# Performance work log

Hardware: AMD Instinct MI355X
Metric: run time of the kernel (lower is better)

The kernel has to match this reference:

```python
import jax, jax.numpy as jnp
import numpy as np

EMBED = 2048
HEADS = 32
HEAD_DIM = EMBED // HEADS
Q_BITS = 4
Q_MAX = 2 ** (Q_BITS - 1) - 1  # 7
DECOMP = 8
CHUNK = 256


def _sym_qdq(x, scale):
    # sym_quant followed by sym_dequant (float32 math, clamp to [-8, 7])
    s = jnp.clip(jnp.abs(scale), 1e-9, None)
    return jnp.clip(jnp.round(x / s), -(Q_MAX + 1), Q_MAX) * s


def _quant_weight(w):
    # per-output-channel symmetric int4 quant-dequant of weight [out, in]
    w = w.astype(jnp.float32)
    s = jnp.max(jnp.abs(w), axis=-1, keepdims=True) / Q_MAX
    return _sym_qdq(w, s)


def _chunk_decompose(x2d):
    """Tender chunked activation quantization.
    Splits rows into chunks of CHUNK, subtracts per-chunk channel bias,
    groups channels into DECOMP scale groups by their column max, and
    applies per-group int4 quant-dequant. Vectorized over the DECOMP groups
    (the masks partition channels, so a per-channel scale gather is exact).
    """
    T, H = x2d.shape
    chunks = (T + CHUNK - 1) // CHUNK
    pad = chunks * CHUNK - T
    xp = jnp.pad(x2d, ((0, pad), (0, 0))).reshape(chunks, CHUNK, H).astype(jnp.float32)
    ch_bias = (jnp.max(xp, axis=1, keepdims=True) + jnp.min(xp, axis=1, keepdims=True)) / 2
    xz = xp - ch_bias                                   # [chunks, CHUNK, H]
    tmax = jnp.max(jnp.abs(xz), axis=(1, 2))            # [chunks]
    cmax = jnp.max(jnp.abs(xz), axis=1)                 # [chunks, H]
    # thresholds t_i = tmax / 2^(DECOMP-1-i), ascending in i
    thr = tmax[:, None] / (2.0 ** jnp.arange(DECOMP - 1, -1, -1, dtype=jnp.float32))
    # group index: i=0 if cmax<=t0, else first i with t_{i-1} < cmax <= t_i
    idx = jnp.sum(cmax[:, :, None] > thr[:, None, : DECOMP - 1], axis=-1)  # [chunks, H]
    scale = tmax[:, None] / (2.0 ** (DECOMP - 1 - idx).astype(jnp.float32)) / Q_MAX
    result = _sym_qdq(xz, scale[:, None, :])            # [chunks, CHUNK, H]
    return result, ch_bias, T


def reference(hidden_states, q_weight, k_weight, v_weight, o_weight,
              q_bias, k_bias, v_bias, o_bias):
    bsz, tgt, H = hidden_states.shape
    # int4 dequantized weights, transposed for right-multiply
    WQ = _quant_weight(q_weight).T
    WK = _quant_weight(k_weight).T
    WV = _quant_weight(v_weight).T
    WO = _quant_weight(o_weight).T

    result, ch_bias, n = _chunk_decompose(hidden_states.reshape(bsz * tgt, H))

    def proj(w_orig, w_dq_t, b):
        # bias-corrected dequant GEMM: per-chunk channel bias uses the
        # ORIGINAL (fp) weight, quantized residual uses the int4 weight
        y = result @ w_dq_t + ch_bias @ w_orig.astype(jnp.float32).T
        return y.reshape(-1, H)[:n] + b

    scaling = HEAD_DIM ** -0.5
    Q = (proj(q_weight, WQ, q_bias) * scaling).reshape(bsz, tgt, HEADS, HEAD_DIM)
    K = proj(k_weight, WK, k_bias).reshape(bsz, tgt, HEADS, HEAD_DIM)
    V = proj(v_weight, WV, v_bias).reshape(bsz, tgt, HEADS, HEAD_DIM)

    # quant_mha == False path: plain attention
    attn = jnp.einsum('bqhd,bkhd->bhqk', Q, K)
    probs = jax.nn.softmax(attn, axis=-1)
    ctx = jnp.einsum('bhqk,bkhd->bqhd', probs, V).reshape(bsz * tgt, H)

    # output projection through the same chunked quant pipeline
    r2, cb2, n2 = _chunk_decompose(ctx)
    out = (r2 @ WO + cb2 @ o_weight.astype(jnp.float32).T).reshape(-1, H)[:n2] + o_bias
    return out.reshape(bsz, tgt, H)


def setup_inputs() -> dict:
    key = jax.random.key(0)
    ks = jax.random.split(key, 10)
    B, T = 2, 1024
    inp = {
        'hidden_states': jax.random.normal(ks[0], (B, T, EMBED), dtype=jnp.float32),
        'q_weight': jax.random.normal(ks[1], (EMBED, EMBED), dtype=jnp.float32) * 0.02,
        'k_weight': jax.random.normal(ks[2], (EMBED, EMBED), dtype=jnp.float32) * 0.02,
        'v_weight': jax.random.normal(ks[3], (EMBED, EMBED), dtype=jnp.float32) * 0.02,
        'o_weight': jax.random.normal(ks[4], (EMBED, EMBED), dtype=jnp.float32) * 0.02,
        'q_bias': jax.random.normal(ks[5], (EMBED,), dtype=jnp.float32) * 0.02,
        'k_bias': jax.random.normal(ks[6], (EMBED,), dtype=jnp.float32) * 0.02,
        'v_bias': jax.random.normal(ks[7], (EMBED,), dtype=jnp.float32) * 0.02,
        'o_bias': jax.random.normal(ks[8], (EMBED,), dtype=jnp.float32) * 0.02,
    }
    return inp
```

## Files before the change

kernel.cpp:

```cpp
#include <hip/hip_runtime.h>
#include <hip/hip_bf16.h>

typedef unsigned short u16;
typedef unsigned int u32;
typedef __attribute__((ext_vector_type(8))) short bs8;
typedef __attribute__((ext_vector_type(4))) float fx4;
typedef __attribute__((ext_vector_type(4))) float f4_t;
typedef __attribute__((ext_vector_type(4))) unsigned int u4_t;

#define HDIM 2048
#define NCH 8

__device__ inline u16 f2bf(float f) {
  __hip_bfloat16 h = __float2bfloat16(f);
  return __builtin_bit_cast(u16, h);
}
__device__ inline float bf2f(u16 u) {
  __hip_bfloat16 h = __builtin_bit_cast(__hip_bfloat16, u);
  return __bfloat162float(h);
}
__device__ inline float pow2i(int e) {
  return __builtin_bit_cast(float, (unsigned)((127 + e) << 23));
}
__device__ inline void gld_lds16(const void* g, void* l) {
  __builtin_amdgcn_global_load_lds((const __attribute__((address_space(1))) void*)g,
                                   (__attribute__((address_space(3))) void*)l, 16, 0, 0);
}

__global__ __launch_bounds__(256) void k_wquant_cbw(
    const float* __restrict__ w0, const float* __restrict__ w1,
    const float* __restrict__ w2, const float* __restrict__ bias,
    u16* __restrict__ wq, float* __restrict__ sw, float* __restrict__ cbw,
    int NC) {
  int o = blockIdx.x, t = threadIdx.x;
  const float* w = (o < 2048) ? w0 : ((o < 4096) ? w1 : w2);
  const float* wrow = w + (size_t)(o & 2047) * HDIM;
  const f4_t* row4 = (const f4_t*)wrow;
  f4_t x0 = row4[2 * t], x1 = row4[2 * t + 1];
  float am = 0.f;
#pragma unroll
  for (int j = 0; j < 4; j++) { am = fmaxf(am, fabsf(x0[j])); am = fmaxf(am, fabsf(x1[j])); }
#pragma unroll
  for (int m = 1; m < 64; m <<= 1) am = fmaxf(am, __shfl_xor(am, m));
  __shared__ float red[4];
  if ((t & 63) == 0) red[t >> 6] = am;
  __syncthreads();
  am = fmaxf(fmaxf(red[0], red[1]), fmaxf(red[2], red[3]));
  float s = fmaxf(am / 7.0f, 1e-9f);
  if (t == 0) sw[o] = s;
  bs8 ov;
#pragma unroll
  for (int j = 0; j < 4; j++) {
    float q0 = fminf(fmaxf(rintf(x0[j] / s), -8.f), 7.f);
    float q1 = fminf(fmaxf(rintf(x1[j] / s), -8.f), 7.f);
    ov[j]     = (short)f2bf(q0);
    ov[j + 4] = (short)f2bf(q1);
  }
  ((bs8*)(wq + (size_t)o * HDIM))[t] = ov;
  float acc[NCH];
#pragma unroll
  for (int c = 0; c < NCH; c++) {
    const f4_t* bc = (const f4_t*)(bias + (size_t)c * HDIM);
    f4_t b0 = bc[2 * t], b1 = bc[2 * t + 1];
    float a = 0.f;
#pragma unroll
    for (int j = 0; j < 4; j++) a += x0[j] * b0[j] + x1[j] * b1[j];
    acc[c] = a;
  }
  __shared__ float redc[NCH][4];
#pragma unroll
  for (int c = 0; c < NCH; c++) {
    float a = acc[c];
#pragma unroll
    for (int m = 1; m < 64; m <<= 1) a += __shfl_xor(a, m);
    if ((t & 63) == 0) redc[c][t >> 6] = a;
  }
  __syncthreads();
  if (t < NCH) cbw[t * NC + o] = redc[t][0] + redc[t][1] + redc[t][2] + redc[t][3];
}

__global__ __launch_bounds__(256) void k_stats(const float* __restrict__ x,
                                               float* __restrict__ biasO,
                                               float* __restrict__ cmaxO) {
  int ch = blockIdx.x >> 3;
  int c = ((blockIdx.x & 7) << 8) + threadIdx.x;
  const float* base = x + (size_t)ch * 256 * HDIM + c;
  float mx = -1e30f, mn = 1e30f;
  for (int r = 0; r < 256; r++) { float v = base[(size_t)r * HDIM]; mx = fmaxf(mx, v); mn = fminf(mn, v); }
  float bi = (mx + mn) * 0.5f;
  biasO[ch * HDIM + c] = bi;
  cmaxO[ch * HDIM + c] = fmaxf(mx - bi, bi - mn);
}

__global__ __launch_bounds__(256) void k_tscale(const float* __restrict__ cmax,
                                                float* __restrict__ scaleO,
                                                float* __restrict__ e2O,
                                                float* __restrict__ tcO) {
  int ch = blockIdx.x, t = threadIdx.x;
  const float* cr = cmax + ch * HDIM;
  float v[8];
  float mx = 0.f;
#pragma unroll
  for (int i = 0; i < 8; i++) { v[i] = cr[i * 256 + t]; mx = fmaxf(mx, v[i]); }
#pragma unroll
  for (int m = 1; m < 64; m <<= 1) mx = fmaxf(mx, __shfl_xor(mx, m));
  __shared__ float red[4];
  __shared__ float tms;
  if ((t & 63) == 0) red[t >> 6] = mx;
  __syncthreads();
  if (t == 0) tms = fmaxf(fmaxf(red[0], red[1]), fmaxf(red[2], red[3]));
  __syncthreads();
  float tmax = tms;
  if (t == 0) tcO[ch] = (tmax / 7.0f) * pow2i(-7);
#pragma unroll
  for (int i = 0; i < 8; i++) {
    int idx = 0;
#pragma unroll
    for (int k = 0; k < 7; k++) idx += (v[i] > tmax * pow2i(k - 7)) ? 1 : 0;
    float s = (tmax * pow2i(idx - 7)) / 7.0f;
    scaleO[ch * HDIM + i * 256 + t] = fmaxf(s, 1e-9f);
    e2O[ch * HDIM + i * 256 + t] = pow2i(idx);
  }
}

__global__ __launch_bounds__(256) void k_qdq(const float* __restrict__ x,
                                             const float* __restrict__ bias,
                                             const float* __restrict__ scale,
                                             const float* __restrict__ e2,
                                             u16* __restrict__ out) {
  int row = blockIdx.x, t = threadIdx.x;
  int ch = row >> 8;
  const f4_t* xr = (const f4_t*)(x + (size_t)row * HDIM);
  const f4_t* br = (const f4_t*)(bias + (size_t)ch * HDIM);
  const f4_t* sr = (const f4_t*)(scale + (size_t)ch * HDIM);
  const f4_t* er = (const f4_t*)(e2 + (size_t)ch * HDIM);
  f4_t x0 = xr[2 * t], x1 = xr[2 * t + 1];
  f4_t b0 = br[2 * t], b1 = br[2 * t + 1];
  f4_t s0 = sr[2 * t], s1 = sr[2 * t + 1];
  f4_t e0 = er[2 * t], e1 = er[2 * t + 1];
  bs8 ov;
#pragma unroll
  for (int j = 0; j < 4; j++) {
    float q0 = fminf(fmaxf(rintf((x0[j] - b0[j]) / s0[j]), -8.f), 7.f);
    ov[j] = (short)f2bf(q0 * e0[j]);
    float q1 = fminf(fmaxf(rintf((x1[j] - b1[j]) / s1[j]), -8.f), 7.f);
    ov[j + 4] = (short)f2bf(q1 * e1[j]);
  }
  ((bs8*)(out + (size_t)row * HDIM))[t] = ov;
}

__global__ __launch_bounds__(256) void k_gemm(
    const u16* __restrict__ A, const u16* __restrict__ B,
    float* __restrict__ o0, float* __restrict__ o1, float* __restrict__ o2,
    const float* __restrict__ cbw, int NC,
    const float* __restrict__ bb0, const float* __restrict__ bb1,
    const float* __restrict__ bb2,
    const float* __restrict__ tc, const float* __restrict__ sw,
    float scl0, float scl1, float scl2) {
  __shared__ u16 smA[128 * 32];
  __shared__ u16 smB[128 * 32];
  int tid = threadIdx.x;
  int wave = tid >> 6, lane = tid & 63;
  int wr = wave >> 1, wc = wave & 1;
  int row0 = blockIdx.y * 128, col0 = blockIdx.x * 128;
  int mat = col0 >> 11;
  float* out = (mat == 0) ? o0 : ((mat == 1) ? o1 : o2);
  const float* bias = (mat == 0) ? bb0 : ((mat == 1) ? bb1 : bb2);
  float scl = (mat == 0) ? scl0 : ((mat == 1) ? scl1 : scl2);
  int chunk = row0 >> 8;
  fx4 zz = {0.f, 0.f, 0.f, 0.f};
  fx4 acc[4][4];
#pragma unroll
  for (int m = 0; m < 4; m++)
#pragma unroll
    for (int n = 0; n < 4; n++) acc[m][n] = zz;

  int offB = wave * 1024 + lane * 16;
  int sr0 = offB >> 6;
  int sr1 = sr0 + 64;
  int sk = (lane & 3) << 3;
  char* ldsA0 = (char*)smA + wave * 1024;
  char* ldsA1 = (char*)smA + 4096 + wave * 1024;
  char* ldsB0 = (char*)smB + wave * 1024;
  char* ldsB1 = (char*)smB + 4096 + wave * 1024;
  const u16* Ab = A + (size_t)row0 * HDIM;
  const u16* Bb = B + (size_t)col0 * HDIM;

  int arow = wr * 64 + (lane & 15);
  int brow = wc * 64 + (lane & 15);
  int kByte = (lane >> 4) << 4;

  for (int kt = 0; kt < HDIM / 32; kt++) {
    int kb = kt * 32 + sk;
    gld_lds16(Ab + (size_t)sr0 * HDIM + kb, ldsA0);
    gld_lds16(Ab + (size_t)sr1 * HDIM + kb, ldsA1);
    gld_lds16(Bb + (size_t)sr0 * HDIM + kb, ldsB0);
    gld_lds16(Bb + (size_t)sr1 * HDIM + kb, ldsB1);
    __syncthreads();
    bs8 af[4], bfr[4];
#pragma unroll
    for (int m = 0; m < 4; m++)
      af[m] = *(const bs8*)((const char*)smA + (size_t)((arow + m * 16) * 64 + kByte));
#pragma unroll
    for (int n = 0; n < 4; n++)
      bfr[n] = *(const bs8*)((const char*)smB + (size_t)((brow + n * 16) * 64 + kByte));
#pragma unroll
    for (int m = 0; m < 4; m++)
#pragma unroll
      for (int n = 0; n < 4; n++)
        acc[m][n] = __builtin_amdgcn_mfma_f32_16x16x32_bf16(af[m], bfr[n], acc[m][n], 0, 0, 0);
    __syncthreads();
  }
  float tcv = tc[chunk];
  int colb = col0 + wc * 64 + (lane & 15);
  int rowb = row0 + wr * 64 + ((lane >> 4) << 2);
#pragma unroll
  for (int m = 0; m < 4; m++) {
#pragma unroll
    for (int n = 0; n < 4; n++) {
      int colg = colb + n * 16;
      int colL = colg - (mat << 11);
      float sc = tcv * sw[colg];
      float cb = cbw[chunk * NC + colg] + bias[colL];
#pragma unroll
      for (int j = 0; j < 4; j++) {
        int row = rowb + m * 16 + j;
        out[(size_t)row * HDIM + colL] = (acc[m][n][j] * sc + cb) * scl;
      }
    }
  }
}

__global__ __launch_bounds__(256) void k_gemm_sk(const u16* __restrict__ A,
                                                 const u16* __restrict__ B,
                                                 float* __restrict__ pbuf) {
  __shared__ u16 smA[128 * 32];
  __shared__ u16 smB[128 * 32];
  int tid = threadIdx.x;
  int wave = tid >> 6, lane = tid & 63;
  int wr = wave >> 1, wc = wave & 1;
  int row0 = blockIdx.y * 128, col0 = blockIdx.x * 128;
  int z = blockIdx.z;
  float* out = pbuf + (size_t)z * HDIM * HDIM;
  fx4 zz = {0.f, 0.f, 0.f, 0.f};
  fx4 acc[4][4];
#pragma unroll
  for (int m = 0; m < 4; m++)
#pragma unroll
    for (int n = 0; n < 4; n++) acc[m][n] = zz;

  int offB = wave * 1024 + lane * 16;
  int sr0 = offB >> 6;
  int sr1 = sr0 + 64;
  int sk = (lane & 3) << 3;
  char* ldsA0 = (char*)smA + wave * 1024;
  char* ldsA1 = (char*)smA + 4096 + wave * 1024;
  char* ldsB0 = (char*)smB + wave * 1024;
  char* ldsB1 = (char*)smB + 4096 + wave * 1024;
  const u16* Ab = A + (size_t)row0 * HDIM;
  const u16* Bb = B + (size_t)col0 * HDIM;

  int arow = wr * 64 + (lane & 15);
  int brow = wc * 64 + (lane & 15);
  int kByte = (lane >> 4) << 4;

  for (int kt = z * 32; kt < z * 32 + 32; kt++) {
    int kb = kt * 32 + sk;
    gld_lds16(Ab + (size_t)sr0 * HDIM + kb, ldsA0);
    gld_lds16(Ab + (size_t)sr1 * HDIM + kb, ldsA1);
    gld_lds16(Bb + (size_t)sr0 * HDIM + kb, ldsB0);
    gld_lds16(Bb + (size_t)sr1 * HDIM + kb, ldsB1);
    __syncthreads();
    bs8 af[4], bfr[4];
#pragma unroll
    for (int m = 0; m < 4; m++)
      af[m] = *(const bs8*)((const char*)smA + (size_t)((arow + m * 16) * 64 + kByte));
#pragma unroll
    for (int n = 0; n < 4; n++)
      bfr[n] = *(const bs8*)((const char*)smB + (size_t)((brow + n * 16) * 64 + kByte));
#pragma unroll
    for (int m = 0; m < 4; m++)
#pragma unroll
      for (int n = 0; n < 4; n++)
        acc[m][n] = __builtin_amdgcn_mfma_f32_16x16x32_bf16(af[m], bfr[n], acc[m][n], 0, 0, 0);
    __syncthreads();
  }
  int colb = col0 + wc * 64 + (lane & 15);
  int rowb = row0 + wr * 64 + ((lane >> 4) << 2);
#pragma unroll
  for (int m = 0; m < 4; m++)
#pragma unroll
    for (int n = 0; n < 4; n++)
#pragma unroll
      for (int j = 0; j < 4; j++)
        out[(size_t)(rowb + m * 16 + j) * HDIM + colb + n * 16] = acc[m][n][j];
}

__global__ __launch_bounds__(256) void k_fin(const float* __restrict__ p0,
                                             const float* __restrict__ p1,
                                             const float* __restrict__ cbw,
                                             const float* __restrict__ bias,
                                             const float* __restrict__ tc,
                                             const float* __restrict__ sw,
                                             float* __restrict__ out) {
  int row = blockIdx.x, t = threadIdx.x;
  int chunk = row >> 8;
  float tcv = tc[chunk];
  const f4_t* a = (const f4_t*)(p0 + (size_t)row * HDIM);
  const f4_t* b = (const f4_t*)(p1 + (size_t)row * HDIM);
  f4_t* o = (f4_t*)(out + (size_t)row * HDIM);
#pragma unroll
  for (int u = 0; u < 2; u++) {
    f4_t x = a[2 * t + u], y = b[2 * t + u];
    f4_t r;
#pragma unroll
    for (int j = 0; j < 4; j++) {
      int c = (2 * t + u) * 4 + j;
      float sc = tcv * sw[c];
      float cb = cbw[chunk * HDIM + c] + bias[c];
      r[j] = ((x[j] + y[j]) * sc + cb) * 1.0f;
    }
    o[2 * t + u] = r;
  }
}

__global__ __launch_bounds__(256) void k_split(const float* __restrict__ Kf,
                                               const float* __restrict__ Vf,
                                               u16* __restrict__ Khg,
                                               u16* __restrict__ Klg,
                                               u16* __restrict__ Vhg,
                                               u16* __restrict__ Vlg) {
  __shared__ u16 Th[4096], Tl[4096];
  int t = threadIdx.x;
  int ti = blockIdx.x & 15, h = (blockIdx.x >> 4) & 31, b = blockIdx.x >> 9;
  size_t rowStart = (size_t)b * 1024 + ti * 64;
  int colh = h * 64;
  size_t tbase = ((size_t)((b * 32 + h) * 16 + ti)) * 4096;
  int kr = t >> 2, d0 = (t & 3) << 4;
  int xk = (kr & 7) << 3;
  const float* kp = Kf + (rowStart + kr) * HDIM + colh + d0;
  const float* vp = Vf + (rowStart + kr) * HDIM + colh + d0;
  f4_t kv[4], vv[4];
#pragma unroll
  for (int qd = 0; qd < 4; qd++) { kv[qd] = *(const f4_t*)(kp + 4 * qd); vv[qd] = *(const f4_t*)(vp + 4 * qd); }
  bs8 h0, l0, h1, l1;
#pragma unroll
  for (int j = 0; j < 4; j++) {
    float x = kv[0][j]; u16 hh = f2bf(x); h0[j] = (short)hh; l0[j] = (short)f2bf(x - bf2f(hh));
    x = kv[1][j]; hh = f2bf(x); h0[j + 4] = (short)hh; l0[j + 4] = (short)f2bf(x - bf2f(hh));
    x = kv[2][j]; hh = f2bf(x); h1[j] = (short)hh; l1[j] = (short)f2bf(x - bf2f(hh));
    x = kv[3][j]; hh = f2bf(x); h1[j + 4] = (short)hh; l1[j + 4] = (short)f2bf(x - bf2f(hh));
  }
  *(bs8*)(Khg + tbase + kr * 64 + (d0 ^ xk)) = h0;
  *(bs8*)(Klg + tbase + kr * 64 + (d0 ^ xk)) = l0;
  *(bs8*)(Khg + tbase + kr * 64 + ((d0 + 8) ^ xk)) = h1;
  *(bs8*)(Klg + tbase + kr * 64 + ((d0 + 8) ^ xk)) = l1;
#pragma unroll
  for (int qd = 0; qd < 4; qd++)
#pragma unroll
    for (int j = 0; j < 4; j++) {
      int d = d0 + 4 * qd + j;
      float x = vv[qd][j]; u16 hh = f2bf(x);
      int vi = d * 64 + (kr ^ ((d & 7) << 3));
      Th[vi] = hh; Tl[vi] = f2bf(x - bf2f(hh));
    }
  __syncthreads();
  *(bs8*)(Vhg + tbase + t * 16) = *(const bs8*)&Th[t * 16];
  *(bs8*)(Vhg + tbase + t * 16 + 8) = *(const bs8*)&Th[t * 16 + 8];
  *(bs8*)(Vlg + tbase + t * 16) = *(const bs8*)&Tl[t * 16];
  *(bs8*)(Vlg + tbase + t * 16 + 8) = *(const bs8*)&Tl[t * 16 + 8];
}

__global__ __launch_bounds__(256) void k_attn(const float* __restrict__ Q,
                                              const u16* __restrict__ Khg,
                                              const u16* __restrict__ Klg,
                                              const u16* __restrict__ Vhg,
                                              const u16* __restrict__ Vlg,
                                              float* __restrict__ O) {
  __shared__ u16 Kh[64 * 64], Kl[64 * 64];
  __shared__ u16 Vh[64 * 64], Vl[64 * 64];
  int tid = threadIdx.x, wave = tid >> 6, lane = tid & 63;
  int l15 = lane & 15, l4 = lane >> 4;
  int lid = blockIdx.x;
  int xcd = lid & 7, jj = lid >> 3;
  int pair = xcd * 8 + (jj >> 3);
  int qt = jj & 7;
  int h = pair & 31, b = pair >> 5;
  size_t rowStart = (size_t)b * 1024;
  int colh = h * 64;
  size_t hbase = (size_t)pair * 16 * 4096;

  bs8 qh[2][2], ql[2][2];
#pragma unroll
  for (int m = 0; m < 2; m++)
#pragma unroll
    for (int kk = 0; kk < 2; kk++) {
      const float* qp = Q + (rowStart + qt * 128 + m * 64 + wave * 16 + l15) * HDIM +
                        colh + kk * 32 + (l4 << 3);
      f4_t a0 = *(const f4_t*)qp;
      f4_t a1 = *(const f4_t*)(qp + 4);
#pragma unroll
      for (int j = 0; j < 4; j++) {
        float x = a0[j]; u16 hh = f2bf(x);
        qh[m][kk][j] = (short)hh; ql[m][kk][j] = (short)f2bf(x - bf2f(hh));
        x = a1[j]; hh = f2bf(x);
        qh[m][kk][j + 4] = (short)hh; ql[m][kk][j + 4] = (short)f2bf(x - bf2f(hh));
      }
    }

  fx4 zz = {0.f, 0.f, 0.f, 0.f};
  fx4 oacc[2][4];
  float mrun[2] = {-1e30f, -1e30f}, lrun[2] = {0.f, 0.f};
#pragma unroll
  for (int m = 0; m < 2; m++)
#pragma unroll
    for (int n = 0; n < 4; n++) oacc[m][n] = zz;

  const u16* garr = (wave == 0) ? Khg : (wave == 1) ? Klg : (wave == 2) ? Vhg : Vlg;
  u16* larr = (wave == 0) ? Kh : (wave == 1) ? Kl : (wave == 2) ? Vh : Vl;

  int srcA = l15 + ((lane & 16) << 1);
  int srcB = srcA + 16;
  int hiSel = l4 >> 1;

  for (int ti = 0; ti < 16; ti++) {
    const u16* gsrc = garr + hbase + (size_t)ti * 4096 + lane * 8;
#pragma unroll
    for (int seg = 0; seg < 8; seg++)
      gld_lds16(gsrc + seg * 512, larr + seg * 512);
    __syncthreads();

    fx4 sf[2][4];
#pragma unroll
    for (int m = 0; m < 2; m++)
#pragma unroll
      for (int n = 0; n < 4; n++) sf[m][n] = zz;
    __builtin_amdgcn_s_setprio(1);
#pragma unroll
    for (int kk = 0; kk < 2; kk++) {
      int colr = kk * 32 + (l4 << 3);
#pragma unroll
      for (int n = 0; n < 4; n++) {
        int row = n * 16 + l15;
        int ko = row * 64 + (colr ^ ((row & 7) << 3));
        bs8 bh = *(const bs8*)&Kh[ko];
        bs8 bl = *(const bs8*)&Kl[ko];
#pragma unroll
        for (int m = 0; m < 2; m++) {
          sf[m][n] = __builtin_amdgcn_mfma_f32_16x16x32_bf16(bl, ql[m][kk], sf[m][n], 0, 0, 0);
          sf[m][n] = __builtin_amdgcn_mfma_f32_16x16x32_bf16(bh, ql[m][kk], sf[m][n], 0, 0, 0);
          sf[m][n] = __builtin_amdgcn_mfma_f32_16x16x32_bf16(bl, qh[m][kk], sf[m][n], 0, 0, 0);
          sf[m][n] = __builtin_amdgcn_mfma_f32_16x16x32_bf16(bh, qh[m][kk], sf[m][n], 0, 0, 0);
        }
      }
    }
    __builtin_amdgcn_s_setprio(0);
    bs8 ph[2][2], pl[2][2];
#pragma unroll
    for (int m = 0; m < 2; m++) {
      float tm = sf[m][0][0];
#pragma unroll
      for (int n = 0; n < 4; n++)
#pragma unroll
        for (int j = 0; j < 4; j++) tm = fmaxf(tm, sf[m][n][j]);
      tm = fmaxf(tm, __shfl_xor(tm, 16));
      tm = fmaxf(tm, __shfl_xor(tm, 32));
      float mn = fmaxf(mrun[m], tm);
      float corr = __expf(mrun[m] - mn);
      mrun[m] = mn;
      float rs = 0.f;
#pragma unroll
      for (int n = 0; n < 4; n++)
#pragma unroll
        for (int j = 0; j < 4; j++) { float p = __expf(sf[m][n][j] - mn); sf[m][n][j] = p; rs += p; }
      rs += __shfl_xor(rs, 16);
      rs += __shfl_xor(rs, 32);
      lrun[m] = lrun[m] * corr + rs;
#pragma unroll
      for (int n = 0; n < 4; n++)
#pragma unroll
        for (int j = 0; j < 4; j++) oacc[m][n][j] *= corr;

      u32 hiw[4][2], low[4][2];
#pragma unroll
      for (int n = 0; n < 4; n++) {
        u16 hh0 = f2bf(sf[m][n][0]), hh1 = f2bf(sf[m][n][1]);
        u16 hh2 = f2bf(sf[m][n][2]), hh3 = f2bf(sf[m][n][3]);
        u16 ll0 = f2bf(sf[m][n][0] - bf2f(hh0)), ll1 = f2bf(sf[m][n][1] - bf2f(hh1));
        u16 ll2 = f2bf(sf[m][n][2] - bf2f(hh2)), ll3 = f2bf(sf[m][n][3] - bf2f(hh3));
        hiw[n][0] = (u32)hh0 | ((u32)hh1 << 16);
        hiw[n][1] = (u32)hh2 | ((u32)hh3 << 16);
        low[n][0] = (u32)ll0 | ((u32)ll1 << 16);
        low[n][1] = (u32)ll2 | ((u32)ll3 << 16);
      }
#pragma unroll
      for (int kkv = 0; kkv < 2; kkv++) {
        u4_t wh, wl;
#pragma unroll
        for (int half = 0; half < 2; half++) {
          int src = half ? srcB : srcA;
#pragma unroll
          for (int pr = 0; pr < 2; pr++) {
            int a0 = __shfl((int)hiw[2 * kkv][pr], src);
            int a1 = __shfl((int)hiw[2 * kkv + 1][pr], src);
            wh[half * 2 + pr] = (u32)(hiSel ? a1 : a0);
            int b0 = __shfl((int)low[2 * kkv][pr], src);
            int b1 = __shfl((int)low[2 * kkv + 1][pr], src);
            wl[half * 2 + pr] = (u32)(hiSel ? b1 : b0);
          }
        }
        ph[m][kkv] = __builtin_bit_cast(bs8, wh);
        pl[m][kkv] = __builtin_bit_cast(bs8, wl);
      }
    }

    __builtin_amdgcn_s_setprio(1);
#pragma unroll
    for (int kkv = 0; kkv < 2; kkv++) {
      int colr = kkv * 32 + (l4 << 3);
#pragma unroll
      for (int n = 0; n < 4; n++) {
        int vrow = n * 16 + l15;
        int vo = vrow * 64 + (colr ^ ((vrow & 7) << 3));
        bs8 vh = *(const bs8*)&Vh[vo];
        bs8 vl = *(const bs8*)&Vl[vo];
#pragma unroll
        for (int m = 0; m < 2; m++) {
          oacc[m][n] = __builtin_amdgcn_mfma_f32_16x16x32_bf16(vl, pl[m][kkv], oacc[m][n], 0, 0, 0);
          oacc[m][n] = __builtin_amdgcn_mfma_f32_16x16x32_bf16(vh, pl[m][kkv], oacc[m][n], 0, 0, 0);
          oacc[m][n] = __builtin_amdgcn_mfma_f32_16x16x32_bf16(vl, ph[m][kkv], oacc[m][n], 0, 0, 0);
          oacc[m][n] = __builtin_amdgcn_mfma_f32_16x16x32_bf16(vh, ph[m][kkv], oacc[m][n], 0, 0, 0);
        }
      }
    }
    __builtin_amdgcn_s_setprio(0);
    __syncthreads();
  }
#pragma unroll
  for (int m = 0; m < 2; m++) {
    size_t token = rowStart + qt * 128 + m * 64 + wave * 16 + l15;
#pragma unroll
    for (int n = 0; n < 4; n++) {
      f4_t r;
#pragma unroll
      for (int j = 0; j < 4; j++) r[j] = oacc[m][n][j] / lrun[m];
      *(f4_t*)(O + token * HDIM + colh + n * 16 + (l4 << 2)) = r;
    }
  }
}

extern "C" void kernel_launch(void* const* d_in, const int* in_sizes, int n_in,
                              void* d_out, int out_size, void* d_ws, size_t ws_size,
                              hipStream_t stream) {
  const float* hs = (const float*)d_in[0];
  const float* qw = (const float*)d_in[1];
  const float* kw = (const float*)d_in[2];
  const float* vw = (const float*)d_in[3];
  const float* ow = (const float*)d_in[4];
  const float* qb = (const float*)d_in[5];
  const float* kb = (const float*)d_in[6];
  const float* vb = (const float*)d_in[7];
  const float* ob = (const float*)d_in[8];

  char* ws = (char*)d_ws;
  const size_t MB = 1u << 20;
  u16* wqQKV = (u16*)(ws + 0 * MB);
  u16* actA  = (u16*)(ws + 24 * MB);
  u16* Khg   = (u16*)(ws + 0 * MB);
  u16* Klg   = (u16*)(ws + 8 * MB);
  u16* Vhg   = (u16*)(ws + 16 * MB);
  u16* Vlg   = (u16*)(ws + 24 * MB);
  float* p01 = (float*)(ws + 0 * MB);
  float* Qf  = (float*)(ws + 32 * MB);
  float* Kf  = (float*)(ws + 48 * MB);
  float* Vf  = (float*)(ws + 64 * MB);
  u16* actA2 = (u16*)(ws + 48 * MB);
  u16* wqO   = (u16*)(ws + 64 * MB);
  float* sm  = (float*)(ws + 80 * MB);
  float* bias1  = sm;
  float* cmax1  = bias1 + NCH * HDIM;
  float* scale1 = cmax1 + NCH * HDIM;
  float* e2_1   = scale1 + NCH * HDIM;
  float* bias2  = e2_1 + NCH * HDIM;
  float* cmax2  = bias2 + NCH * HDIM;
  float* scale2 = cmax2 + NCH * HDIM;
  float* e2_2   = scale2 + NCH * HDIM;
  float* cbwQKV = e2_2 + NCH * HDIM;
  float* swQKV  = cbwQKV + NCH * 3 * HDIM;
  float* cbwO   = swQKV + 3 * HDIM;
  float* swO    = cbwO + NCH * HDIM;
  float* tc1    = swO + HDIM;
  float* tc2    = tc1 + NCH;
  float* ctx = (float*)d_out;

  k_stats<<<64, 256, 0, stream>>>(hs, bias1, cmax1);
  k_tscale<<<8, 256, 0, stream>>>(cmax1, scale1, e2_1, tc1);
  k_qdq<<<2048, 256, 0, stream>>>(hs, bias1, scale1, e2_1, actA);
  k_wquant_cbw<<<6144, 256, 0, stream>>>(qw, kw, vw, bias1, wqQKV, swQKV, cbwQKV, 3 * HDIM);
  k_gemm<<<dim3(48, 16), 256, 0, stream>>>(actA, wqQKV, Qf, Kf, Vf,
                                           cbwQKV, 3 * HDIM, qb, kb, vb,
                                           tc1, swQKV, 0.125f, 1.0f, 1.0f);
  k_split<<<1024, 256, 0, stream>>>(Kf, Vf, Khg, Klg, Vhg, Vlg);
  k_attn<<<512, 256, 0, stream>>>(Qf, Khg, Klg, Vhg, Vlg, ctx);
  k_stats<<<64, 256, 0, stream>>>(ctx, bias2, cmax2);
  k_tscale<<<8, 256, 0, stream>>>(cmax2, scale2, e2_2, tc2);
  k_qdq<<<2048, 256, 0, stream>>>(ctx, bias2, scale2, e2_2, actA2);
  k_wquant_cbw<<<2048, 256, 0, stream>>>(ow, ow, ow, bias2, wqO, swO, cbwO, HDIM);
  k_gemm_sk<<<dim3(16, 16, 2), 256, 0, stream>>>(actA2, wqO, p01);
  k_fin<<<2048, 256, 0, stream>>>(p01, p01 + (size_t)HDIM * HDIM,
                                  cbwO, ob, tc2, swO, (float*)d_out);
}
```

Measured before the change: 297.9 us.

## Fuse K/V bf16 split into QKV GEMM, double-buffer attention tiles, 3-way split-K

The separate k_split kernel is removed. The QKV GEMM epilogue now writes K and V directly as swizzled hi/lo bf16 tiles, so the fp32 K/V intermediates are never written to or read back from global memory. The cost is scattered 2-byte stores in the epilogue instead of coalesced fp32 rows. The attention kernel gains LDS double buffering so the next K/V tile is prefetched while the current one is computed, at the cost of doubling its LDS use. The output-projection split-K goes from 2 to 3 slices, with one partial staged in the output buffer, to fill more CUs; this adds one more partial to write and read.

```diff
diff --git a/kernel.cpp b/kernel.cpp
--- a/kernel.cpp
+++ b/kernel.cpp
@@ -149,14 +149,15 @@
   ((bs8*)(out + (size_t)row * HDIM))[t] = ov;
 }
 
-__global__ __launch_bounds__(256) void k_gemm(
+__global__ __launch_bounds__(256) void k_gemm_qkv(
     const u16* __restrict__ A, const u16* __restrict__ B,
-    float* __restrict__ o0, float* __restrict__ o1, float* __restrict__ o2,
-    const float* __restrict__ cbw, int NC,
+    float* __restrict__ Qf,
+    u16* __restrict__ Khg, u16* __restrict__ Klg,
+    u16* __restrict__ Vhg, u16* __restrict__ Vlg,
+    const float* __restrict__ cbw,
     const float* __restrict__ bb0, const float* __restrict__ bb1,
     const float* __restrict__ bb2,
-    const float* __restrict__ tc, const float* __restrict__ sw,
-    float scl0, float scl1, float scl2) {
+    const float* __restrict__ tc, const float* __restrict__ sw) {
   __shared__ u16 smA[128 * 32];
   __shared__ u16 smB[128 * 32];
   int tid = threadIdx.x;
@@ -164,9 +165,8 @@
   int wr = wave >> 1, wc = wave & 1;
   int row0 = blockIdx.y * 128, col0 = blockIdx.x * 128;
   int mat = col0 >> 11;
-  float* out = (mat == 0) ? o0 : ((mat == 1) ? o1 : o2);
   const float* bias = (mat == 0) ? bb0 : ((mat == 1) ? bb1 : bb2);
-  float scl = (mat == 0) ? scl0 : ((mat == 1) ? scl1 : scl2);
+  float scl = (mat == 0) ? 0.125f : 1.0f;
   int chunk = row0 >> 8;
   fx4 zz = {0.f, 0.f, 0.f, 0.f};
   fx4 acc[4][4];
@@ -219,13 +219,29 @@
 #pragma unroll
     for (int n = 0; n < 4; n++) {
       int colg = colb + n * 16;
-      int colL = colg - (mat << 11);
+      int colL = colg & 2047;
       float sc = tcv * sw[colg];
-      float cb = cbw[chunk * NC + colg] + bias[colL];
+      float cb = cbw[chunk * (3 * HDIM) + colg] + bias[colL];
 #pragma unroll
       for (int j = 0; j < 4; j++) {
         int row = rowb + m * 16 + j;
-        out[(size_t)row * HDIM + colL] = (acc[m][n][j] * sc + cb) * scl;
+        float y = (acc[m][n][j] * sc + cb) * scl;
+        if (mat == 0) {
+          Qf[(size_t)row * HDIM + colL] = y;
+        } else {
+          u16 hh = f2bf(y);
+          u16 ll = f2bf(y - bf2f(hh));
+          int d = colL & 63, hd = colL >> 6;
+          int bb_ = row >> 10, ti = (row >> 6) & 15, kr = row & 63;
+          size_t tbase = ((size_t)(((bb_ << 5) + hd) * 16 + ti)) << 12;
+          if (mat == 1) {
+            size_t a_ = tbase + kr * 64 + (d ^ ((kr & 7) << 3));
+            Khg[a_] = hh; Klg[a_] = ll;
+          } else {
+            size_t a_ = tbase + d * 64 + (kr ^ ((d & 7) << 3));
+            Vhg[a_] = hh; Vlg[a_] = ll;
+          }
+        }
       }
     }
   }
@@ -233,7 +249,9 @@
 
 __global__ __launch_bounds__(256) void k_gemm_sk(const u16* __restrict__ A,
                                                  const u16* __restrict__ B,
-                                                 float* __restrict__ pbuf) {
+                                                 float* __restrict__ p0,
+                                                 float* __restrict__ p1,
+                                                 float* __restrict__ p2) {
   __shared__ u16 smA[128 * 32];
   __shared__ u16 smB[128 * 32];
   int tid = threadIdx.x;
@@ -241,7 +259,9 @@
   int wr = wave >> 1, wc = wave & 1;
   int row0 = blockIdx.y * 128, col0 = blockIdx.x * 128;
   int z = blockIdx.z;
-  float* out = pbuf + (size_t)z * HDIM * HDIM;
+  float* out = (z == 0) ? p0 : ((z == 1) ? p1 : p2);
+  int kt0 = 21 * z;
+  int kt1 = (z == 2) ? 64 : (21 * z + 21);
   fx4 zz = {0.f, 0.f, 0.f, 0.f};
   fx4 acc[4][4];
 #pragma unroll
@@ -264,7 +284,7 @@
   int brow = wc * 64 + (lane & 15);
   int kByte = (lane >> 4) << 4;
 
-  for (int kt = z * 32; kt < z * 32 + 32; kt++) {
+  for (int kt = kt0; kt < kt1; kt++) {
     int kb = kt * 32 + sk;
     gld_lds16(Ab + (size_t)sr0 * HDIM + kb, ldsA0);
     gld_lds16(Ab + (size_t)sr1 * HDIM + kb, ldsA1);
@@ -298,6 +318,7 @@
 
 __global__ __launch_bounds__(256) void k_fin(const float* __restrict__ p0,
                                              const float* __restrict__ p1,
+                                             const float* __restrict__ p2,
                                              const float* __restrict__ cbw,
                                              const float* __restrict__ bias,
                                              const float* __restrict__ tc,
@@ -308,67 +329,21 @@
   float tcv = tc[chunk];
   const f4_t* a = (const f4_t*)(p0 + (size_t)row * HDIM);
   const f4_t* b = (const f4_t*)(p1 + (size_t)row * HDIM);
+  const f4_t* c_ = (const f4_t*)(p2 + (size_t)row * HDIM);
   f4_t* o = (f4_t*)(out + (size_t)row * HDIM);
 #pragma unroll
   for (int u = 0; u < 2; u++) {
-    f4_t x = a[2 * t + u], y = b[2 * t + u];
+    f4_t x = a[2 * t + u], y = b[2 * t + u], w = c_[2 * t + u];
     f4_t r;
 #pragma unroll
     for (int j = 0; j < 4; j++) {
       int c = (2 * t + u) * 4 + j;
       float sc = tcv * sw[c];
       float cb = cbw[chunk * HDIM + c] + bias[c];
-      r[j] = ((x[j] + y[j]) * sc + cb) * 1.0f;
+      r[j] = ((x[j] + y[j] + w[j]) * sc + cb) * 1.0f;
     }
     o[2 * t + u] = r;
   }
-}
-
-__global__ __launch_bounds__(256) void k_split(const float* __restrict__ Kf,
-                                               const float* __restrict__ Vf,
-                                               u16* __restrict__ Khg,
-                                               u16* __restrict__ Klg,
-                                               u16* __restrict__ Vhg,
-                                               u16* __restrict__ Vlg) {
-  __shared__ u16 Th[4096], Tl[4096];
-  int t = threadIdx.x;
-  int ti = blockIdx.x & 15, h = (blockIdx.x >> 4) & 31, b = blockIdx.x >> 9;
-  size_t rowStart = (size_t)b * 1024 + ti * 64;
-  int colh = h * 64;
-  size_t tbase = ((size_t)((b * 32 + h) * 16 + ti)) * 4096;
-  int kr = t >> 2, d0 = (t & 3) << 4;
-  int xk = (kr & 7) << 3;
-  const float* kp = Kf + (rowStart + kr) * HDIM + colh + d0;
-  const float* vp = Vf + (rowStart + kr) * HDIM + colh + d0;
-  f4_t kv[4], vv[4];
-#pragma unroll
-  for (int qd = 0; qd < 4; qd++) { kv[qd] = *(const f4_t*)(kp + 4 * qd); vv[qd] = *(const f4_t*)(vp + 4 * qd); }
-  bs8 h0, l0, h1, l1;
-#pragma unroll
-  for (int j = 0; j < 4; j++) {
-    float x = kv[0][j]; u16 hh = f2bf(x); h0[j] = (short)hh; l0[j] = (short)f2bf(x - bf2f(hh));
-    x = kv[1][j]; hh = f2bf(x); h0[j + 4] = (short)hh; l0[j + 4] = (short)f2bf(x - bf2f(hh));
-    x = kv[2][j]; hh = f2bf(x); h1[j] = (short)hh; l1[j] = (short)f2bf(x - bf2f(hh));
-    x = kv[3][j]; hh = f2bf(x); h1[j + 4] = (short)hh; l1[j + 4] = (short)f2bf(x - bf2f(hh));
-  }
-  *(bs8*)(Khg + tbase + kr * 64 + (d0 ^ xk)) = h0;
-  *(bs8*)(Klg + tbase + kr * 64 + (d0 ^ xk)) = l0;
-  *(bs8*)(Khg + tbase + kr * 64 + ((d0 + 8) ^ xk)) = h1;
-  *(bs8*)(Klg + tbase + kr * 64 + ((d0 + 8) ^ xk)) = l1;
-#pragma unroll
-  for (int qd = 0; qd < 4; qd++)
-#pragma unroll
-    for (int j = 0; j < 4; j++) {
-      int d = d0 + 4 * qd + j;
-      float x = vv[qd][j]; u16 hh = f2bf(x);
-      int vi = d * 64 + (kr ^ ((d & 7) << 3));
-      Th[vi] = hh; Tl[vi] = f2bf(x - bf2f(hh));
-    }
-  __syncthreads();
-  *(bs8*)(Vhg + tbase + t * 16) = *(const bs8*)&Th[t * 16];
-  *(bs8*)(Vhg + tbase + t * 16 + 8) = *(const bs8*)&Th[t * 16 + 8];
-  *(bs8*)(Vlg + tbase + t * 16) = *(const bs8*)&Tl[t * 16];
-  *(bs8*)(Vlg + tbase + t * 16 + 8) = *(const bs8*)&Tl[t * 16 + 8];
 }
 
 __global__ __launch_bounds__(256) void k_attn(const float* __restrict__ Q,
@@ -377,8 +352,8 @@
                                               const u16* __restrict__ Vhg,
                                               const u16* __restrict__ Vlg,
                                               float* __restrict__ O) {
-  __shared__ u16 Kh[64 * 64], Kl[64 * 64];
-  __shared__ u16 Vh[64 * 64], Vl[64 * 64];
+  __shared__ u16 KhB[2][4096], KlB[2][4096];
+  __shared__ u16 VhB[2][4096], VlB[2][4096];
   int tid = threadIdx.x, wave = tid >> 6, lane = tid & 63;
   int l15 = lane & 15, l4 = lane >> 4;
   int lid = blockIdx.x;
@@ -417,18 +392,34 @@
     for (int n = 0; n < 4; n++) oacc[m][n] = zz;
 
   const u16* garr = (wave == 0) ? Khg : (wave == 1) ? Klg : (wave == 2) ? Vhg : Vlg;
-  u16* larr = (wave == 0) ? Kh : (wave == 1) ? Kl : (wave == 2) ? Vh : Vl;
+  u16* larr0 = (wave == 0) ? KhB[0] : (wave == 1) ? KlB[0] : (wave == 2) ? VhB[0] : VlB[0];
+  u16* larr1 = (wave == 0) ? KhB[1] : (wave == 1) ? KlB[1] : (wave == 2) ? VhB[1] : VlB[1];
 
   int srcA = l15 + ((lane & 16) << 1);
   int srcB = srcA + 16;
   int hiSel = l4 >> 1;
 
+  {
+    const u16* gsrc = garr + hbase + lane * 8;
+#pragma unroll
+    for (int seg = 0; seg < 8; seg++)
+      gld_lds16(gsrc + seg * 512, larr0 + seg * 512);
+  }
+  __syncthreads();
+
   for (int ti = 0; ti < 16; ti++) {
-    const u16* gsrc = garr + hbase + (size_t)ti * 4096 + lane * 8;
-#pragma unroll
-    for (int seg = 0; seg < 8; seg++)
-      gld_lds16(gsrc + seg * 512, larr + seg * 512);
-    __syncthreads();
+    int cur = ti & 1;
+    if (ti + 1 < 16) {
+      const u16* gsrc = garr + hbase + (size_t)(ti + 1) * 4096 + lane * 8;
+      u16* dst = cur ? larr0 : larr1;
+#pragma unroll
+      for (int seg = 0; seg < 8; seg++)
+        gld_lds16(gsrc + seg * 512, dst + seg * 512);
+    }
+    const u16* KhC = cur ? KhB[1] : KhB[0];
+    const u16* KlC = cur ? KlB[1] : KlB[0];
+    const u16* VhC = cur ? VhB[1] : VhB[0];
+    const u16* VlC = cur ? VlB[1] : VlB[0];
 
     fx4 sf[2][4];
 #pragma unroll
@@ -443,8 +434,8 @@
       for (int n = 0; n < 4; n++) {
         int row = n * 16 + l15;
         int ko = row * 64 + (colr ^ ((row & 7) << 3));
-        bs8 bh = *(const bs8*)&Kh[ko];
-        bs8 bl = *(const bs8*)&Kl[ko];
+        bs8 bh = *(const bs8*)&KhC[ko];
+        bs8 bl = *(const bs8*)&KlC[ko];
 #pragma unroll
         for (int m = 0; m < 2; m++) {
           sf[m][n] = __builtin_amdgcn_mfma_f32_16x16x32_bf16(bl, ql[m][kk], sf[m][n], 0, 0, 0);
@@ -522,8 +513,8 @@
       for (int n = 0; n < 4; n++) {
         int vrow = n * 16 + l15;
         int vo = vrow * 64 + (colr ^ ((vrow & 7) << 3));
-        bs8 vh = *(const bs8*)&Vh[vo];
-        bs8 vl = *(const bs8*)&Vl[vo];
+        bs8 vh = *(const bs8*)&VhC[vo];
+        bs8 vl = *(const bs8*)&VlC[vo];
 #pragma unroll
         for (int m = 0; m < 2; m++) {
           oacc[m][n] = __builtin_amdgcn_mfma_f32_16x16x32_bf16(vl, pl[m][kkv], oacc[m][n], 0, 0, 0);
@@ -566,16 +557,15 @@
   const size_t MB = 1u << 20;
   u16* wqQKV = (u16*)(ws + 0 * MB);
   u16* actA  = (u16*)(ws + 24 * MB);
-  u16* Khg   = (u16*)(ws + 0 * MB);
-  u16* Klg   = (u16*)(ws + 8 * MB);
-  u16* Vhg   = (u16*)(ws + 16 * MB);
-  u16* Vlg   = (u16*)(ws + 24 * MB);
-  float* p01 = (float*)(ws + 0 * MB);
+  float* p0  = (float*)(ws + 0 * MB);
+  float* p1  = (float*)(ws + 16 * MB);
   float* Qf  = (float*)(ws + 32 * MB);
-  float* Kf  = (float*)(ws + 48 * MB);
-  float* Vf  = (float*)(ws + 64 * MB);
+  u16* Khg   = (u16*)(ws + 48 * MB);
+  u16* Klg   = (u16*)(ws + 56 * MB);
+  u16* Vhg   = (u16*)(ws + 64 * MB);
+  u16* Vlg   = (u16*)(ws + 72 * MB);
   u16* actA2 = (u16*)(ws + 48 * MB);
-  u16* wqO   = (u16*)(ws + 64 * MB);
+  u16* wqO   = (u16*)(ws + 56 * MB);
   float* sm  = (float*)(ws + 80 * MB);
   float* bias1  = sm;
   float* cmax1  = bias1 + NCH * HDIM;
@@ -592,21 +582,19 @@
   float* tc1    = swO + HDIM;
   float* tc2    = tc1 + NCH;
   float* ctx = (float*)d_out;
+  float* p2  = (float*)d_out;
 
   k_stats<<<64, 256, 0, stream>>>(hs, bias1, cmax1);
   k_tscale<<<8, 256, 0, stream>>>(cmax1, scale1, e2_1, tc1);
   k_qdq<<<2048, 256, 0, stream>>>(hs, bias1, scale1, e2_1, actA);
   k_wquant_cbw<<<6144, 256, 0, stream>>>(qw, kw, vw, bias1, wqQKV, swQKV, cbwQKV, 3 * HDIM);
-  k_gemm<<<dim3(48, 16), 256, 0, stream>>>(actA, wqQKV, Qf, Kf, Vf,
-                                           cbwQKV, 3 * HDIM, qb, kb, vb,
-                                           tc1, swQKV, 0.125f, 1.0f, 1.0f);
-  k_split<<<1024, 256, 0, stream>>>(Kf, Vf, Khg, Klg, Vhg, Vlg);
+  k_gemm_qkv<<<dim3(48, 16), 256, 0, stream>>>(actA, wqQKV, Qf, Khg, Klg, Vhg, Vlg,
+                                               cbwQKV, qb, kb, vb, tc1, swQKV);
   k_attn<<<512, 256, 0, stream>>>(Qf, Khg, Klg, Vhg, Vlg, ctx);
   k_stats<<<64, 256, 0, stream>>>(ctx, bias2, cmax2);
   k_tscale<<<8, 256, 0, stream>>>(cmax2, scale2, e2_2, tc2);
   k_qdq<<<2048, 256, 0, stream>>>(ctx, bias2, scale2, e2_2, actA2);
   k_wquant_cbw<<<2048, 256, 0, stream>>>(ow, ow, ow, bias2, wqO, swO, cbwO, HDIM);
-  k_gemm_sk<<<dim3(16, 16, 2), 256, 0, stream>>>(actA2, wqO, p01);
-  k_fin<<<2048, 256, 0, stream>>>(p01, p01 + (size_t)HDIM * HDIM,
-                                  cbwO, ob, tc2, swO, (float*)d_out);
-}
+  k_gemm_sk<<<dim3(16, 16, 3), 256, 0, stream>>>(actA2, wqO, p0, p1, p2);
+  k_fin<<<2048, 256, 0, stream>>>(p0, p1, p2, cbwO, ob, tc2, swO, (float*)d_out);
+}
```

Measured after the change: 311.5 us. 1.05x slower.
